# Performance work log

Measured on AMD Instinct MI355X. Metric: run time of the kernel, lower is better.

The kernel has to match this reference:

```python
import jax, jax.numpy as jnp
import numpy as np

DIM = 128
B, N = 4, 4096


def setup_inputs() -> dict:
    key = jax.random.key(0)
    k1, k2, k3 = jax.random.split(key, 3)
    return {
        "key": jax.random.normal(k1, (B, N, DIM), dtype=jnp.float32),
        "query": jax.random.normal(k2, (B, N, DIM), dtype=jnp.float32),
        "value": jax.random.normal(k3, (B, N, DIM), dtype=jnp.float32),
    }


def reference(key, query, value):
    # score[b, i, j] = <query[b, i], key[b, j]> / sqrt(dim)
    inv_sqrt_dim = 1.0 / jnp.sqrt(jnp.float32(DIM))
    score = jnp.einsum("bqd,bkd->bqk", query, key) * inv_sqrt_dim
    attn = jax.nn.softmax(score, axis=-1)
    context = jnp.einsum("bqk,bkd->bqd", attn, value)
    return (context, attn)
```

## Files before the change

### kernel.cpp

```cpp
#include <hip/hip_runtime.h>
#include <hip/hip_bf16.h>

#define BDIM 4
#define NSEQ 4096
#define DHEAD 128
#define SCALE 0.08838834764831845f

typedef __bf16 bf16x8 __attribute__((ext_vector_type(8)));
typedef float f32x4 __attribute__((ext_vector_type(4)));
typedef float f32x16 __attribute__((ext_vector_type(16)));
typedef unsigned int u32x4 __attribute__((ext_vector_type(4)));

__device__ __forceinline__ unsigned short f2bf(float f){
    return __builtin_bit_cast(unsigned short, (__bf16)f);
}
__device__ __forceinline__ unsigned long long pack4(float4 u){
    return (unsigned long long)f2bf(u.x)
         | ((unsigned long long)f2bf(u.y) << 16)
         | ((unsigned long long)f2bf(u.z) << 32)
         | ((unsigned long long)f2bf(u.w) << 48);
}
__device__ __forceinline__ void gload_lds16(const void* g, void* l){
    __builtin_amdgcn_global_load_lds(
        (const __attribute__((address_space(1))) unsigned int*)g,
        (__attribute__((address_space(3))) unsigned int*)l, 16, 0, 0);
}

extern "C" __global__ __launch_bounds__(256, 4)
void stats_repack(const float* __restrict__ K, const float* __restrict__ Q,
                  const float* __restrict__ V, char* __restrict__ ws)
{
    const int bid0 = blockIdx.x;
    const int tid = threadIdx.x;

    if (bid0 >= 1024) {
        const int rid = bid0 - 1024;
        const int T = rid & 127;
        const int b = rid >> 7;

        char* Kp = ws + ((size_t)(b * 128 + T) << 14);
        const float* Ks = K + ((size_t)b * NSEQ + T * 32) * DHEAD;
        const float* Vs = V + ((size_t)b * NSEQ + T * 32) * DHEAD;

#pragma unroll
        for (int i = 0; i < 2; i++) {
            int u = tid + 256 * i;
            int ds = u >> 6, ln = u & 63;
            int m = ln & 31, hi = ln >> 5;
            const float* s = Ks + (size_t)m * DHEAD + ds * 16 + hi * 8;
            float4 a = *(const float4*)s;
            float4 bq = *(const float4*)(s + 4);
            ulonglong2 wv;
            wv.x = pack4(a);
            wv.y = pack4(bq);
            *(ulonglong2*)(Kp + u * 16) = wv;
        }
#pragma unroll
        for (int i = 0; i < 2; i++) {
            int u = tid + 256 * i;
            int f = u >> 6, ln = u & 63;
            int dg = f >> 1, kb = f & 1;
            int dd = ln & 31, hi = ln >> 5;
            int d = dg * 32 + dd;
            const float* s = Vs + (size_t)(kb * 16 + hi * 8) * DHEAD + d;
            float v0 = s[0 * DHEAD], v1 = s[1 * DHEAD], v2 = s[2 * DHEAD], v3 = s[3 * DHEAD];
            float v4 = s[4 * DHEAD], v5 = s[5 * DHEAD], v6 = s[6 * DHEAD], v7 = s[7 * DHEAD];
            ulonglong2 wv;
            wv.x = (unsigned long long)f2bf(v0)
                 | ((unsigned long long)f2bf(v1) << 16)
                 | ((unsigned long long)f2bf(v2) << 32)
                 | ((unsigned long long)f2bf(v3) << 48);
            wv.y = (unsigned long long)f2bf(v4)
                 | ((unsigned long long)f2bf(v5) << 16)
                 | ((unsigned long long)f2bf(v6) << 32)
                 | ((unsigned long long)f2bf(v7) << 48);
            *(ulonglong2*)(Kp + 8192 + u * 16) = wv;
        }
        return;
    }

    __shared__ __align__(16) char Klds[64 * 256];

    float* pbase = (float*)(ws + (8u << 20));
    const int bid = bid0;
    const int ks  = bid & 3;
    const int rt  = (bid >> 2) & 63;
    const int b   = bid >> 8;
    const int lane = tid & 63;
    const int w    = tid >> 6;
    const int g    = lane >> 4;
    const int c    = lane & 15;
    const int rowbase = rt * 64;

    const float* qrow = Q + ((size_t)b * NSEQ + rowbase + w * 16 + c) * DHEAD;
    bf16x8 qf[4];
#pragma unroll
    for (int kk = 0; kk < 4; kk++) {
        const float4* p0 = (const float4*)(qrow + g * 8 + kk * 32);
        float4 u = p0[0], v = p0[1];
        bf16x8 t;
        t[0] = (__bf16)(u.x * SCALE); t[1] = (__bf16)(u.y * SCALE);
        t[2] = (__bf16)(u.z * SCALE); t[3] = (__bf16)(u.w * SCALE);
        t[4] = (__bf16)(v.x * SCALE); t[5] = (__bf16)(v.y * SCALE);
        t[6] = (__bf16)(v.z * SCALE); t[7] = (__bf16)(v.w * SCALE);
        qf[kk] = t;
    }

    float m[4], l[4];
#pragma unroll
    for (int r = 0; r < 4; r++) { m[r] = -1e30f; l[r] = 0.0f; }

    const int f  = tid & 31;
    const int r0 = tid >> 5;

    for (int kt = 0; kt < 16; kt++) {
        const float* ktile = K + ((size_t)b * NSEQ + ks * 1024 + kt * 64) * DHEAD;
#pragma unroll
        for (int i = 0; i < 8; i++) {
            int r = r0 + i * 8;
            float4 u = *(const float4*)(ktile + (size_t)r * DHEAD + f * 4);
            *(unsigned long long*)(Klds + r * 256 + ((f * 8) ^ ((r & 7) << 4))) = pack4(u);
        }
        __syncthreads();

        f32x4 acc[4];
#pragma unroll
        for (int n = 0; n < 4; n++) acc[n] = (f32x4){0.f, 0.f, 0.f, 0.f};
#pragma unroll
        for (int n = 0; n < 4; n++) {
            int row = n * 16 + c;
#pragma unroll
            for (int kk = 0; kk < 4; kk++) {
                bf16x8 kf = *(const bf16x8*)(Klds + row * 256 +
                                ((g * 16 + kk * 64) ^ ((row & 7) << 4)));
                acc[n] = __builtin_amdgcn_mfma_f32_16x16x32_bf16(qf[kk], kf, acc[n], 0, 0, 0);
            }
        }

#pragma unroll
        for (int r = 0; r < 4; r++) {
            float t = fmaxf(fmaxf(acc[0][r], acc[1][r]), fmaxf(acc[2][r], acc[3][r]));
            t = fmaxf(t, __shfl_xor(t, 1));
            t = fmaxf(t, __shfl_xor(t, 2));
            t = fmaxf(t, __shfl_xor(t, 4));
            t = fmaxf(t, __shfl_xor(t, 8));
            float mn = fmaxf(m[r], t);
            float sc = __expf(m[r] - mn);
            float ps = __expf(acc[0][r] - mn) + __expf(acc[1][r] - mn)
                     + __expf(acc[2][r] - mn) + __expf(acc[3][r] - mn);
            ps += __shfl_xor(ps, 1);
            ps += __shfl_xor(ps, 2);
            ps += __shfl_xor(ps, 4);
            ps += __shfl_xor(ps, 8);
            l[r] = l[r] * sc + ps;
            m[r] = mn;
        }
        __syncthreads();
    }

    if (c == 0) {
#pragma unroll
        for (int r = 0; r < 4; r++) {
            size_t row = rowbase + w * 16 + g * 4 + r;
            float* p = pbase + ((size_t)b * NSEQ + row) * 8 + ks * 2;
            p[0] = m[r];
            p[1] = l[r];
        }
    }
}

extern "C" __global__ __launch_bounds__(256, 3)
void attn_mf2(const char* __restrict__ ws, const float* __restrict__ Q,
              float* __restrict__ out, float* __restrict__ part)
{
    __shared__ __align__(16) char LDS[32768];

    const int bid = blockIdx.x;
    const int ks  = bid & 7;
    const int qt  = (bid >> 3) & 31;
    const int b   = bid >> 8;
    const int tid = threadIdx.x;
    const int wv  = tid >> 6;
    const int lane = tid & 63;
    const int hi   = lane >> 5;
    const int qq   = lane & 31;
    const int q    = qt * 128 + wv * 32 + qq;

    float* attn = out + (size_t)BDIM * NSEQ * DHEAD;
    const float* pb = (const float*)(ws + (8u << 20));

    float Cq;
    {
        const float* prow = pb + ((size_t)b * NSEQ + q) * 8;
        float4 p0 = *(const float4*)prow;
        float4 p1 = *(const float4*)(prow + 4);
        float M = fmaxf(fmaxf(p0.x, p0.z), fmaxf(p1.x, p1.z));
        float L = p0.y * __expf(p0.x - M) + p0.w * __expf(p0.z - M)
                + p1.y * __expf(p1.x - M) + p1.w * __expf(p1.z - M);
        Cq = M + __logf(L);
    }

    const float* qrow = Q + ((size_t)b * NSEQ + q) * DHEAD;
    bf16x8 qf[8];
#pragma unroll
    for (int ds = 0; ds < 8; ds++) {
        const float4* p0 = (const float4*)(qrow + ds * 16 + hi * 8);
        float4 u = p0[0], v = p0[1];
        bf16x8 t;
        t[0] = (__bf16)(u.x * SCALE); t[1] = (__bf16)(u.y * SCALE);
        t[2] = (__bf16)(u.z * SCALE); t[3] = (__bf16)(u.w * SCALE);
        t[4] = (__bf16)(v.x * SCALE); t[5] = (__bf16)(v.y * SCALE);
        t[6] = (__bf16)(v.z * SCALE); t[7] = (__bf16)(v.w * SCALE);
        qf[ds] = t;
    }

    f32x16 ctx[4];
#pragma unroll
    for (int dg = 0; dg < 4; dg++) ctx[dg] = (f32x16)(0.0f);

    const char* img = ws + ((size_t)(b * 128 + ks * 16) << 14);

#pragma unroll
    for (int i = 0; i < 4; i++) {
        int o = tid * 16 + i * 4096;
        gload_lds16(img + o, LDS + o);
    }

    float* arowb = attn + ((size_t)b * NSEQ + q) * NSEQ + ks * 512 + 4 * hi;

    for (int kt = 0; kt < 16; kt++) {
        __builtin_amdgcn_s_barrier();
        __builtin_amdgcn_sched_barrier(0);
        if (kt < 15) {
            const char* src = img + ((size_t)(kt + 1) << 14);
            char* dst = LDS + (((kt + 1) & 1) << 14);
#pragma unroll
            for (int i = 0; i < 4; i++) {
                int o = tid * 16 + i * 4096;
                gload_lds16(src + o, dst + o);
            }
            asm volatile("s_waitcnt vmcnt(4)" ::: "memory");
        } else {
            asm volatile("s_waitcnt vmcnt(0)" ::: "memory");
        }
        __builtin_amdgcn_s_barrier();
        __builtin_amdgcn_sched_barrier(0);

        const char* bufc = LDS + ((kt & 1) << 14);

        f32x16 s0 = (f32x16)(0.0f), s1 = (f32x16)(0.0f);
        __builtin_amdgcn_s_setprio(1);
#pragma unroll
        for (int dp = 0; dp < 4; dp++) {
            bf16x8 kfa = *(const bf16x8*)(bufc + (2 * dp) * 1024 + lane * 16);
            bf16x8 kfb = *(const bf16x8*)(bufc + (2 * dp + 1) * 1024 + lane * 16);
            s0 = __builtin_amdgcn_mfma_f32_32x32x16_bf16(kfa, qf[2 * dp], s0, 0, 0, 0);
            s1 = __builtin_amdgcn_mfma_f32_32x32x16_bf16(kfb, qf[2 * dp + 1], s1, 0, 0, 0);
        }
        __builtin_amdgcn_s_setprio(0);

        float p[16];
#pragma unroll
        for (int r = 0; r < 16; r++) p[r] = __expf((s0[r] + s1[r]) - Cq);

        float* arow = arowb + kt * 32;
#pragma unroll
        for (int j = 0; j < 4; j++) {
            float4 pv = {p[4 * j], p[4 * j + 1], p[4 * j + 2], p[4 * j + 3]};
            *(float4*)(arow + 8 * j) = pv;
        }

        unsigned int bpk[8], sb[8];
#pragma unroll
        for (int i = 0; i < 8; i++)
            bpk[i] = (unsigned int)f2bf(p[2 * i]) | ((unsigned int)f2bf(p[2 * i + 1]) << 16);
#pragma unroll
        for (int i = 0; i < 8; i++)
            sb[i] = (unsigned int)__shfl_xor((int)bpk[i], 32);

        u32x4 w0, w1;
        w0[0] = hi ? sb[2] : bpk[0];
        w0[1] = hi ? sb[3] : bpk[1];
        w0[2] = hi ? bpk[2] : sb[0];
        w0[3] = hi ? bpk[3] : sb[1];
        w1[0] = hi ? sb[6] : bpk[4];
        w1[1] = hi ? sb[7] : bpk[5];
        w1[2] = hi ? bpk[6] : sb[4];
        w1[3] = hi ? bpk[7] : sb[5];
        bf16x8 pf0 = __builtin_bit_cast(bf16x8, w0);
        bf16x8 pf1 = __builtin_bit_cast(bf16x8, w1);

        __builtin_amdgcn_s_setprio(1);
#pragma unroll
        for (int dg = 0; dg < 4; dg++) {
            bf16x8 vf0 = *(const bf16x8*)(bufc + 8192 + (dg * 2 + 0) * 1024 + lane * 16);
            bf16x8 vf1 = *(const bf16x8*)(bufc + 8192 + (dg * 2 + 1) * 1024 + lane * 16);
            ctx[dg] = __builtin_amdgcn_mfma_f32_32x32x16_bf16(vf0, pf0, ctx[dg], 0, 0, 0);
            ctx[dg] = __builtin_amdgcn_mfma_f32_32x32x16_bf16(vf1, pf1, ctx[dg], 0, 0, 0);
        }
        __builtin_amdgcn_s_setprio(0);
    }

    float* cp = part + (((size_t)(ks * 4 + b) * NSEQ + q) * DHEAD) + 4 * hi;
#pragma unroll
    for (int dg = 0; dg < 4; dg++)
#pragma unroll
        for (int j = 0; j < 4; j++) {
            float4 v = {ctx[dg][4 * j], ctx[dg][4 * j + 1],
                        ctx[dg][4 * j + 2], ctx[dg][4 * j + 3]};
            *(float4*)(cp + dg * 32 + 8 * j) = v;
        }
}

extern "C" __global__ __launch_bounds__(256, 4)
void ctx_reduce8(const float4* __restrict__ part, float4* __restrict__ out)
{
    const size_t gt = (size_t)blockIdx.x * 256 + threadIdx.x;
    const size_t stride = (size_t)BDIM * NSEQ * DHEAD / 4;
    float4 s = part[gt];
#pragma unroll
    for (int i = 1; i < 8; i++) {
        float4 a = part[gt + (size_t)i * stride];
        s.x += a.x; s.y += a.y; s.z += a.z; s.w += a.w;
    }
    out[gt] = s;
}

extern "C" __global__ __launch_bounds__(256, 4)
void attn_stats_fb(const float* __restrict__ K, const float* __restrict__ Q,
                   float* __restrict__ pbase, int pstride)
{
    __shared__ __align__(16) char Klds[64 * 256];

    const int bid = blockIdx.x;
    const int ks  = bid & 3;
    const int rt  = (bid >> 2) & 63;
    const int b   = bid >> 8;
    const int tid = threadIdx.x;
    const int lane = tid & 63;
    const int w    = tid >> 6;
    const int g    = lane >> 4;
    const int c    = lane & 15;
    const int rowbase = rt * 64;

    const float* qrow = Q + ((size_t)b * NSEQ + rowbase + w * 16 + c) * DHEAD;
    bf16x8 qf[4];
#pragma unroll
    for (int kk = 0; kk < 4; kk++) {
        const float4* p0 = (const float4*)(qrow + g * 8 + kk * 32);
        float4 u = p0[0], v = p0[1];
        bf16x8 t;
        t[0] = (__bf16)(u.x * SCALE); t[1] = (__bf16)(u.y * SCALE);
        t[2] = (__bf16)(u.z * SCALE); t[3] = (__bf16)(u.w * SCALE);
        t[4] = (__bf16)(v.x * SCALE); t[5] = (__bf16)(v.y * SCALE);
        t[6] = (__bf16)(v.z * SCALE); t[7] = (__bf16)(v.w * SCALE);
        qf[kk] = t;
    }

    float m[4], l[4];
#pragma unroll
    for (int r = 0; r < 4; r++) { m[r] = -1e30f; l[r] = 0.0f; }

    const int f  = tid & 31;
    const int r0 = tid >> 5;

    for (int kt = 0; kt < 16; kt++) {
        const float* ktile = K + ((size_t)b * NSEQ + ks * 1024 + kt * 64) * DHEAD;
#pragma unroll
        for (int i = 0; i < 8; i++) {
            int r = r0 + i * 8;
            float4 u = *(const float4*)(ktile + (size_t)r * DHEAD + f * 4);
            *(unsigned long long*)(Klds + r * 256 + ((f * 8) ^ ((r & 7) << 4))) = pack4(u);
        }
        __syncthreads();

        f32x4 acc[4];
#pragma unroll
        for (int n = 0; n < 4; n++) acc[n] = (f32x4){0.f, 0.f, 0.f, 0.f};
#pragma unroll
        for (int n = 0; n < 4; n++) {
            int row = n * 16 + c;
#pragma unroll
            for (int kk = 0; kk < 4; kk++) {
                bf16x8 kf = *(const bf16x8*)(Klds + row * 256 +
                                ((g * 16 + kk * 64) ^ ((row & 7) << 4)));
                acc[n] = __builtin_amdgcn_mfma_f32_16x16x32_bf16(qf[kk], kf, acc[n], 0, 0, 0);
            }
        }

#pragma unroll
        for (int r = 0; r < 4; r++) {
            float t = fmaxf(fmaxf(acc[0][r], acc[1][r]), fmaxf(acc[2][r], acc[3][r]));
            t = fmaxf(t, __shfl_xor(t, 1));
            t = fmaxf(t, __shfl_xor(t, 2));
            t = fmaxf(t, __shfl_xor(t, 4));
            t = fmaxf(t, __shfl_xor(t, 8));
            float mn = fmaxf(m[r], t);
            float sc = __expf(m[r] - mn);
            float ps = __expf(acc[0][r] - mn) + __expf(acc[1][r] - mn)
                     + __expf(acc[2][r] - mn) + __expf(acc[3][r] - mn);
            ps += __shfl_xor(ps, 1);
            ps += __shfl_xor(ps, 2);
            ps += __shfl_xor(ps, 4);
            ps += __shfl_xor(ps, 8);
            l[r] = l[r] * sc + ps;
            m[r] = mn;
        }
        __syncthreads();
    }

    if (c == 0) {
#pragma unroll
        for (int r = 0; r < 4; r++) {
            size_t row = rowbase + w * 16 + g * 4 + r;
            float* p = pbase + ((size_t)b * NSEQ + row) * pstride + ks * 2;
            p[0] = m[r];
            p[1] = l[r];
        }
    }
}

extern "C" __global__ __launch_bounds__(512, 2)
void attn_final_fb(const float* __restrict__ K, const float* __restrict__ Q,
                   const float* __restrict__ V, float* __restrict__ out)
{
    __shared__ __align__(16) char LDS[81920];

    const int bid = blockIdx.x;
    const int rt  = bid & 63;
    const int b   = bid >> 6;
    const int tid = threadIdx.x;
    const int rowbase = rt * 64;
    const int lane = tid & 63;
    const int w    = tid >> 6;
    const int rw   = w & 3;
    const int grp  = w >> 2;
    const int g    = lane >> 4;
    const int c    = lane & 15;
    const int t    = tid & 255;

    float* ctxOut = out;
    float* attn   = out + (size_t)BDIM * NSEQ * DHEAD;

    char* Klds  = LDS + grp * 16384;
    char* Vtlds = LDS + 32768 + grp * 16384;
    char* Plds  = LDS + 65536 + w * 2048;

    float Cq;
    {
        const float* prow = attn + ((size_t)b * NSEQ + rowbase + rw * 16 + c) * NSEQ;
        float4 p0 = *(const float4*)prow;
        float4 p1 = *(const float4*)(prow + 4);
        float M = fmaxf(fmaxf(p0.x, p0.z), fmaxf(p1.x, p1.z));
        float L = p0.y * __expf(p0.x - M) + p0.w * __expf(p0.z - M)
                + p1.y * __expf(p1.x - M) + p1.w * __expf(p1.z - M);
        Cq = M + __logf(L);
    }

    const float* qrow = Q + ((size_t)b * NSEQ + rowbase + rw * 16 + c) * DHEAD;
    bf16x8 qf[4];
#pragma unroll
    for (int kk = 0; kk < 4; kk++) {
        const float4* p0 = (const float4*)(qrow + g * 8 + kk * 32);
        float4 u = p0[0], v = p0[1];
        bf16x8 tt;
        tt[0] = (__bf16)(u.x * SCALE); tt[1] = (__bf16)(u.y * SCALE);
        tt[2] = (__bf16)(u.z * SCALE); tt[3] = (__bf16)(u.w * SCALE);
        tt[4] = (__bf16)(v.x * SCALE); tt[5] = (__bf16)(v.y * SCALE);
        tt[6] = (__bf16)(v.z * SCALE); tt[7] = (__bf16)(v.w * SCALE);
        qf[kk] = tt;
    }

    f32x4 ctx[8];
#pragma unroll
    for (int n2 = 0; n2 < 8; n2++) ctx[n2] = (f32x4){0.f, 0.f, 0.f, 0.f};

    __syncthreads();

    const int fK = t & 31;
    const int rK = t >> 5;
    const int dq = t & 15;
    const int kb = t >> 4;
    const int k0 = kb * 4;
    const int d0 = dq * 2;

    const float* kbase = K + ((size_t)b * NSEQ + grp * 2048) * DHEAD;
    const float* vbase = V + ((size_t)b * NSEQ + grp * 2048) * DHEAD;

    float4 kreg[8];
    float2 vreg[4][4];

#pragma unroll
    for (int i = 0; i < 8; i++)
        kreg[i] = *(const float4*)(kbase + (size_t)(rK + i * 8) * DHEAD + fK * 4);
#pragma unroll
    for (int i = 0; i < 4; i++)
#pragma unroll
        for (int j = 0; j < 4; j++)
            vreg[i][j] = *(const float2*)(vbase + (size_t)(k0 + j) * DHEAD + d0 + 32 * i);

    for (int kt = 0; kt < 32; kt++) {
        __builtin_amdgcn_s_barrier();

#pragma unroll
        for (int i = 0; i < 8; i++) {
            int row = rK + i * 8;
            *(unsigned long long*)(Klds + row * 256 + ((fK * 8) ^ ((row & 7) << 4))) = pack4(kreg[i]);
        }
#pragma unroll
        for (int i = 0; i < 4; i++) {
            int d = d0 + 32 * i;
            unsigned long long rr0 =
                (unsigned long long)f2bf(vreg[i][0].x)
              | ((unsigned long long)f2bf(vreg[i][1].x) << 16)
              | ((unsigned long long)f2bf(vreg[i][2].x) << 32)
              | ((unsigned long long)f2bf(vreg[i][3].x) << 48);
            unsigned long long rr1 =
                (unsigned long long)f2bf(vreg[i][0].y)
              | ((unsigned long long)f2bf(vreg[i][1].y) << 16)
              | ((unsigned long long)f2bf(vreg[i][2].y) << 32)
              | ((unsigned long long)f2bf(vreg[i][3].y) << 48);
            int swz = (d & 7) << 4;
            *(unsigned long long*)(Vtlds + d * 128 + ((k0 * 2) ^ swz)) = rr0;
            *(unsigned long long*)(Vtlds + (d + 1) * 128 + ((k0 * 2) ^ (swz + 16))) = rr1;
        }
        asm volatile("s_waitcnt lgkmcnt(0)" ::: "memory");
        __builtin_amdgcn_s_barrier();

        {
            int kn = (kt + 1) & 31;
            const float* kp = kbase + (size_t)kn * 64 * DHEAD;
            const float* vp = vbase + (size_t)kn * 64 * DHEAD;
#pragma unroll
            for (int i = 0; i < 8; i++)
                kreg[i] = *(const float4*)(kp + (size_t)(rK + i * 8) * DHEAD + fK * 4);
#pragma unroll
            for (int i = 0; i < 4; i++)
#pragma unroll
                for (int j = 0; j < 4; j++)
                    vreg[i][j] = *(const float2*)(vp + (size_t)(k0 + j) * DHEAD + d0 + 32 * i);
        }

        f32x4 sacc[4];
#pragma unroll
        for (int nt = 0; nt < 4; nt++) sacc[nt] = (f32x4){0.f, 0.f, 0.f, 0.f};
        __builtin_amdgcn_s_setprio(1);
#pragma unroll
        for (int nt = 0; nt < 4; nt++) {
            int row = nt * 16 + c;
#pragma unroll
            for (int kk = 0; kk < 4; kk++) {
                bf16x8 kf = *(const bf16x8*)(Klds + row * 256 +
                                ((g * 16 + kk * 64) ^ ((row & 7) << 4)));
                sacc[nt] = __builtin_amdgcn_mfma_f32_16x16x32_bf16(kf, qf[kk], sacc[nt], 0, 0, 0);
            }
        }
        __builtin_amdgcn_s_setprio(0);

        const int col0 = grp * 2048 + kt * 64;
        float* arow = attn + ((size_t)b * NSEQ + rowbase + rw * 16 + c) * NSEQ + col0;
#pragma unroll
        for (int nt = 0; nt < 4; nt++) {
            float4 pv;
            pv.x = __expf(sacc[nt][0] - Cq);
            pv.y = __expf(sacc[nt][1] - Cq);
            pv.z = __expf(sacc[nt][2] - Cq);
            pv.w = __expf(sacc[nt][3] - Cq);
            *(float4*)(arow + nt * 16 + g * 4) = pv;
            *(unsigned long long*)(Plds + c * 128 +
                ((nt * 32 + g * 8) ^ ((c & 7) << 4))) = pack4(pv);
        }
        asm volatile("s_waitcnt lgkmcnt(0)" ::: "memory");
        __builtin_amdgcn_sched_barrier(0);

        bf16x8 pf[2];
#pragma unroll
        for (int kk = 0; kk < 2; kk++)
            pf[kk] = *(const bf16x8*)(Plds + c * 128 +
                        ((kk * 64 + g * 16) ^ ((c & 7) << 4)));

        __builtin_amdgcn_s_setprio(1);
#pragma unroll
        for (int n2 = 0; n2 < 8; n2++) {
            int d = n2 * 16 + c;
#pragma unroll
            for (int kk = 0; kk < 2; kk++) {
                bf16x8 vff = *(const bf16x8*)(Vtlds + d * 128 +
                                ((kk * 64 + g * 16) ^ ((d & 7) << 4)));
                ctx[n2] = __builtin_amdgcn_mfma_f32_16x16x32_bf16(pf[kk], vff, ctx[n2], 0, 0, 0);
            }
        }
        __builtin_amdgcn_s_setprio(0);
    }

    __syncthreads();

    float* red = (float*)LDS;
    if (grp == 1) {
#pragma unroll
        for (int n2 = 0; n2 < 8; n2++)
#pragma unroll
            for (int r = 0; r < 4; r++)
                red[(rw * 16 + g * 4 + r) * 128 + n2 * 16 + c] = ctx[n2][r];
    }
    __syncthreads();
    if (grp == 0) {
#pragma unroll
        for (int n2 = 0; n2 < 8; n2++)
#pragma unroll
            for (int r = 0; r < 4; r++) {
                size_t row = rowbase + rw * 16 + g * 4 + r;
                ctxOut[((size_t)b * NSEQ + row) * DHEAD + n2 * 16 + c] =
                    ctx[n2][r] + red[(rw * 16 + g * 4 + r) * 128 + n2 * 16 + c];
            }
    }
}

extern "C" void kernel_launch(void* const* d_in, const int* in_sizes, int n_in,
                              void* d_out, int out_size, void* d_ws, size_t ws_size,
                              hipStream_t stream)
{
    const float* K = (const float*)d_in[0];
    const float* Q = (const float*)d_in[1];
    const float* V = (const float*)d_in[2];
    float* out  = (float*)d_out;
    float* attn = out + (size_t)BDIM * NSEQ * DHEAD;

    const size_t ctx_bytes = (size_t)BDIM * NSEQ * DHEAD * sizeof(float);
    const size_t need      = (9u << 20) + 8 * ctx_bytes;

    if (ws_size >= need) {
        char* ws = (char*)d_ws;
        float* part = (float*)(ws + (9u << 20));
        stats_repack<<<dim3(1024 + 512), dim3(256), 0, stream>>>(K, Q, V, ws);
        attn_mf2<<<dim3(1024), dim3(256), 0, stream>>>(ws, Q, out, part);
        ctx_reduce8<<<dim3(2048), dim3(256), 0, stream>>>((const float4*)part, (float4*)out);
    } else {
        attn_stats_fb<<<dim3(4 * 64 * 4), dim3(256), 0, stream>>>(K, Q, attn, NSEQ);
        attn_final_fb<<<dim3(4 * 64), dim3(512), 0, stream>>>(K, Q, V, out);
    }
}
```

Measured before the change: 155.4 us.

## Fuse split-K context reduction into attention kernel and use exp2 softmax

Removes the separate ctx_reduce8 launch: each attention block writes its partial context and bumps an atomic counter per (query tile, batch), and the last of the eight blocks sums the partials into the output. The log2e factor is folded into the Q scaling and the log-sum-exp constant so that exp2 can be used, packed bf16 conversion uses v_cvt_pk_bf16_f32, the occupancy hint goes from 3 to 4 blocks per CU, and the vmcnt wait is relaxed so that more prefetches stay in flight. This saves a kernel launch and a pass over the partial buffers, at the cost of a memset, fences and an imbalanced tail in which a few blocks do the reduction.

```diff
diff --git a/kernel.cpp b/kernel.cpp
--- a/kernel.cpp
+++ b/kernel.cpp
@@ -5,6 +5,7 @@
 #define NSEQ 4096
 #define DHEAD 128
 #define SCALE 0.08838834764831845f
+#define LOG2E 1.4426950408889634f
 
 typedef __bf16 bf16x8 __attribute__((ext_vector_type(8)));
 typedef float f32x4 __attribute__((ext_vector_type(4)));
@@ -24,6 +25,14 @@
     __builtin_amdgcn_global_load_lds(
         (const __attribute__((address_space(1))) unsigned int*)g,
         (__attribute__((address_space(3))) unsigned int*)l, 16, 0, 0);
+}
+__device__ __forceinline__ unsigned int cvt_pk_bf16(float lo, float hi){
+    unsigned int r;
+    asm("v_cvt_pk_bf16_f32 %0, %1, %2" : "=v"(r) : "v"(lo), "v"(hi));
+    return r;
+}
+__device__ __forceinline__ float fast_exp2(float x){
+    return __builtin_amdgcn_exp2f(x);
 }
 
 extern "C" __global__ __launch_bounds__(256, 4)
@@ -169,11 +178,13 @@
     }
 }
 
-extern "C" __global__ __launch_bounds__(256, 3)
-void attn_mf2(const char* __restrict__ ws, const float* __restrict__ Q,
-              float* __restrict__ out, float* __restrict__ part)
+extern "C" __global__ __launch_bounds__(256, 4)
+void attn_mf3(const char* __restrict__ ws, const float* __restrict__ Q,
+              float* __restrict__ out, float* __restrict__ part,
+              int* __restrict__ cnt)
 {
     __shared__ __align__(16) char LDS[32768];
+    __shared__ int sLast;
 
     const int bid = blockIdx.x;
     const int ks  = bid & 7;
@@ -189,7 +200,7 @@
     float* attn = out + (size_t)BDIM * NSEQ * DHEAD;
     const float* pb = (const float*)(ws + (8u << 20));
 
-    float Cq;
+    float Cq2;
     {
         const float* prow = pb + ((size_t)b * NSEQ + q) * 8;
         float4 p0 = *(const float4*)prow;
@@ -197,20 +208,21 @@
         float M = fmaxf(fmaxf(p0.x, p0.z), fmaxf(p1.x, p1.z));
         float L = p0.y * __expf(p0.x - M) + p0.w * __expf(p0.z - M)
                 + p1.y * __expf(p1.x - M) + p1.w * __expf(p1.z - M);
-        Cq = M + __logf(L);
+        Cq2 = (M + __logf(L)) * LOG2E;
     }
 
     const float* qrow = Q + ((size_t)b * NSEQ + q) * DHEAD;
+    const float QS = SCALE * LOG2E;
     bf16x8 qf[8];
 #pragma unroll
     for (int ds = 0; ds < 8; ds++) {
         const float4* p0 = (const float4*)(qrow + ds * 16 + hi * 8);
         float4 u = p0[0], v = p0[1];
         bf16x8 t;
-        t[0] = (__bf16)(u.x * SCALE); t[1] = (__bf16)(u.y * SCALE);
-        t[2] = (__bf16)(u.z * SCALE); t[3] = (__bf16)(u.w * SCALE);
-        t[4] = (__bf16)(v.x * SCALE); t[5] = (__bf16)(v.y * SCALE);
-        t[6] = (__bf16)(v.z * SCALE); t[7] = (__bf16)(v.w * SCALE);
+        t[0] = (__bf16)(u.x * QS); t[1] = (__bf16)(u.y * QS);
+        t[2] = (__bf16)(u.z * QS); t[3] = (__bf16)(u.w * QS);
+        t[4] = (__bf16)(v.x * QS); t[5] = (__bf16)(v.y * QS);
+        t[6] = (__bf16)(v.z * QS); t[7] = (__bf16)(v.w * QS);
         qf[ds] = t;
     }
 
@@ -239,7 +251,11 @@
                 int o = tid * 16 + i * 4096;
                 gload_lds16(src + o, dst + o);
             }
-            asm volatile("s_waitcnt vmcnt(4)" ::: "memory");
+            if (kt == 0) {
+                asm volatile("s_waitcnt vmcnt(4)" ::: "memory");
+            } else {
+                asm volatile("s_waitcnt vmcnt(8)" ::: "memory");
+            }
         } else {
             asm volatile("s_waitcnt vmcnt(0)" ::: "memory");
         }
@@ -261,7 +277,7 @@
 
         float p[16];
 #pragma unroll
-        for (int r = 0; r < 16; r++) p[r] = __expf((s0[r] + s1[r]) - Cq);
+        for (int r = 0; r < 16; r++) p[r] = fast_exp2((s0[r] + s1[r]) - Cq2);
 
         float* arow = arowb + kt * 32;
 #pragma unroll
@@ -273,7 +289,7 @@
         unsigned int bpk[8], sb[8];
 #pragma unroll
         for (int i = 0; i < 8; i++)
-            bpk[i] = (unsigned int)f2bf(p[2 * i]) | ((unsigned int)f2bf(p[2 * i + 1]) << 16);
+            bpk[i] = cvt_pk_bf16(p[2 * i], p[2 * i + 1]);
 #pragma unroll
         for (int i = 0; i < 8; i++)
             sb[i] = (unsigned int)__shfl_xor((int)bpk[i], 32);
@@ -301,29 +317,41 @@
         __builtin_amdgcn_s_setprio(0);
     }
 
-    float* cp = part + (((size_t)(ks * 4 + b) * NSEQ + q) * DHEAD) + 4 * hi;
-#pragma unroll
-    for (int dg = 0; dg < 4; dg++)
-#pragma unroll
-        for (int j = 0; j < 4; j++) {
-            float4 v = {ctx[dg][4 * j], ctx[dg][4 * j + 1],
-                        ctx[dg][4 * j + 2], ctx[dg][4 * j + 3]};
-            *(float4*)(cp + dg * 32 + 8 * j) = v;
-        }
-}
-
-extern "C" __global__ __launch_bounds__(256, 4)
-void ctx_reduce8(const float4* __restrict__ part, float4* __restrict__ out)
-{
-    const size_t gt = (size_t)blockIdx.x * 256 + threadIdx.x;
-    const size_t stride = (size_t)BDIM * NSEQ * DHEAD / 4;
-    float4 s = part[gt];
-#pragma unroll
-    for (int i = 1; i < 8; i++) {
-        float4 a = part[gt + (size_t)i * stride];
-        s.x += a.x; s.y += a.y; s.z += a.z; s.w += a.w;
-    }
-    out[gt] = s;
+    {
+        float* cp = part + (((size_t)(ks * 4 + b) * NSEQ + q) * DHEAD) + 4 * hi;
+#pragma unroll
+        for (int dg = 0; dg < 4; dg++)
+#pragma unroll
+            for (int j = 0; j < 4; j++) {
+                float4 v = {ctx[dg][4 * j], ctx[dg][4 * j + 1],
+                            ctx[dg][4 * j + 2], ctx[dg][4 * j + 3]};
+                *(float4*)(cp + dg * 32 + 8 * j) = v;
+            }
+    }
+    __threadfence();
+    __syncthreads();
+    if (tid == 0) {
+        int old = atomicAdd(cnt + ((qt << 2) | b), 1);
+        sLast = (old == 7) ? 1 : 0;
+    }
+    __syncthreads();
+    if (sLast) {
+        __threadfence();
+        const float4* p4 = (const float4*)part;
+        float4* o4 = (float4*)out;
+        const size_t base = (size_t)qt * 128 * 32;
+#pragma unroll 4
+        for (int e = 0; e < 16; e++) {
+            size_t g4 = (size_t)tid + 256 * e;
+            float4 s = {0.f, 0.f, 0.f, 0.f};
+#pragma unroll
+            for (int i = 0; i < 8; i++) {
+                float4 a = p4[(size_t)(i * 4 + b) * ((size_t)NSEQ * 32) + base + g4];
+                s.x += a.x; s.y += a.y; s.z += a.z; s.w += a.w;
+            }
+            o4[((size_t)b * NSEQ + (size_t)qt * 128) * 32 + g4] = s;
+        }
+    }
 }
 
 extern "C" __global__ __launch_bounds__(256, 4)
@@ -632,9 +660,10 @@
     if (ws_size >= need) {
         char* ws = (char*)d_ws;
         float* part = (float*)(ws + (9u << 20));
+        int* cnt = (int*)(ws + (8u << 20) + (512u << 10));
+        (void)hipMemsetAsync(cnt, 0, 128 * sizeof(int), stream);
         stats_repack<<<dim3(1024 + 512), dim3(256), 0, stream>>>(K, Q, V, ws);
-        attn_mf2<<<dim3(1024), dim3(256), 0, stream>>>(ws, Q, out, part);
-        ctx_reduce8<<<dim3(2048), dim3(256), 0, stream>>>((const float4*)part, (float4*)out);
+        attn_mf3<<<dim3(1024), dim3(256), 0, stream>>>(ws, Q, out, part, cnt);
     } else {
         attn_stats_fb<<<dim3(4 * 64 * 4), dim3(256), 0, stream>>>(K, Q, attn, NSEQ);
         attn_final_fb<<<dim3(4 * 64), dim3(512), 0, stream>>>(K, Q, V, out);
```

Result: slower. 490.6 us (+215.6%).
